# Performance work log

Measured on AMD Instinct MI355X. Metric: run time of the kernel, lower is better.

Reference implementation:

```python
import jax, jax.numpy as jnp
import numpy as np
from jax import lax

B, CIN, H, W = 64, 1024, 28, 28
MID, COUT = 256, 1024  # mid_channels, out_channels*expansion
EMB = 64
EPS = 1e-5


def _conv(x, w, stride=1, padding='VALID'):
    return lax.conv_general_dilated(
        x, w, window_strides=(stride, stride), padding=padding,
        dimension_numbers=('NCHW', 'OIHW', 'NCHW'))


def _bn(x, gamma, beta):
    # training-mode BatchNorm2d: batch statistics over (N,H,W)
    m = jnp.mean(x, axis=(0, 2, 3), keepdims=True)
    v = jnp.var(x, axis=(0, 2, 3), keepdims=True)
    return (x - m) * lax.rsqrt(v + EPS) * gamma[None, :, None, None] + beta[None, :, None, None]


def setup_inputs() -> dict:
    key = jax.random.key(0)
    ks = jax.random.split(key, 12)
    he = lambda k, shape, fan_in: jax.random.normal(k, shape, jnp.float32) * np.float32(np.sqrt(2.0 / fan_in))
    return {
        'x': jax.random.normal(ks[0], (B, CIN, H, W), jnp.float32),
        'embeddings': jax.random.normal(ks[1], (B, EMB), jnp.float32),
        # sparse gating networks: Linear(emb_dim -> channels) + ReLU
        'w_gate1': he(ks[2], (EMB, MID), EMB), 'b_gate1': jnp.zeros((MID,), jnp.float32),
        'w_gate2': he(ks[3], (EMB, MID), EMB), 'b_gate2': jnp.zeros((MID,), jnp.float32),
        'conv1_w': he(ks[4], (MID, CIN, 1, 1), CIN),
        'bn1_g': jnp.ones((MID,), jnp.float32), 'bn1_b': jnp.zeros((MID,), jnp.float32),
        'conv2_w': he(ks[5], (MID, MID, 3, 3), MID * 9),
        'bn2_g': jnp.ones((MID,), jnp.float32), 'bn2_b': jnp.zeros((MID,), jnp.float32),
        'conv3_w': he(ks[6], (COUT, MID, 1, 1), MID),
        'bn3_g': jnp.ones((COUT,), jnp.float32), 'bn3_b': jnp.zeros((COUT,), jnp.float32),
    }


def reference(x, embeddings, w_gate1, b_gate1, w_gate2, b_gate2,
              conv1_w, bn1_g, bn1_b, conv2_w, bn2_g, bn2_b,
              conv3_w, bn3_g, bn3_b):
    identity = x
    # gate 1: ReLU-sparse gating over mid channels, per sample
    g1 = jax.nn.relu(embeddings @ w_gate1 + b_gate1)            # [B, MID]
    out = _conv(x, conv1_w) * g1[:, :, None, None]              # MoE conv1x1
    out = jax.nn.relu(_bn(out, bn1_g, bn1_b))
    g2 = jax.nn.relu(embeddings @ w_gate2 + b_gate2)            # [B, MID]
    out = _conv(out, conv2_w, stride=1, padding='SAME') * g2[:, :, None, None]  # MoE conv3x3
    out = jax.nn.relu(_bn(out, bn2_g, bn2_b))
    out = _conv(out, conv3_w)                                   # plain conv1x1
    out = _bn(out, bn3_g, bn3_b)
    out = jax.nn.relu(out + identity)
    return out, g1, g2
```

## Files before the change

kernel.cpp:

```cpp
#include <hip/hip_runtime.h>
#include <stdint.h>

#define NB 64
#define CINC 1024
#define HWD 784
#define MIDC 256
#define COUTC 1024
#define EMBD 64

typedef __attribute__((ext_vector_type(8))) short short8;
typedef __attribute__((ext_vector_type(4))) float f32x4;

#define GLOAD16(gp, lp)                                                     \
  __builtin_amdgcn_global_load_lds(                                         \
      (const __attribute__((address_space(1))) void*)(gp),                  \
      (__attribute__((address_space(3))) void*)(lp), 16, 0, 0)

__device__ __forceinline__ ushort f2bf(float f) {
  union { float f; uint32_t u; } v; v.f = f;
  uint32_t r = v.u + 0x7fffu + ((v.u >> 16) & 1u);
  return (ushort)(r >> 16);
}
__device__ __forceinline__ float bf2f(ushort b) {
  union { uint32_t u; float f; } v; v.u = ((uint32_t)b) << 16;
  return v.f;
}
__device__ __forceinline__ uint32_t pack2(float a, float b) {
  return (uint32_t)f2bf(a) | ((uint32_t)f2bf(b) << 16);
}

static const size_t OFF_Y1   = 0;
static const size_t OFF_Y2   = 25690112;
static const size_t OFF_W1   = 51380224;
static const size_t OFF_W3   = 51904512;
static const size_t OFF_W2R  = 52428800;
static const size_t OFF_STAT = 53608448;
static const size_t OFF_PAR  = 53620736;
static const size_t OFF_ZB   = 58720256;

__global__ __launch_bounds__(256) void k_gates(
    const float* __restrict__ emb, const float* __restrict__ w1,
    const float* __restrict__ b1, const float* __restrict__ w2,
    const float* __restrict__ b2, float* __restrict__ out_tail) {
  int b = blockIdx.x, which = blockIdx.y, n = threadIdx.x;
  const float* w = which ? w2 : w1;
  const float* bias = which ? b2 : b1;
  __shared__ float se[EMBD];
  if (n < EMBD) se[n] = emb[b * EMBD + n];
  __syncthreads();
  float acc = bias[n];
#pragma unroll 8
  for (int e = 0; e < EMBD; e++) acc += se[e] * w[e * MIDC + n];
  acc = fmaxf(acc, 0.f);
  out_tail[which * (NB * MIDC) + b * MIDC + n] = acc;
}

__global__ void k_repack(const float* __restrict__ w1, const float* __restrict__ w2,
                         const float* __restrict__ w3, ushort* __restrict__ W1b,
                         ushort* __restrict__ W2r, ushort* __restrict__ W3b) {
  int total = 262144 + 262144 + 589824;
  for (int i = blockIdx.x * blockDim.x + threadIdx.x; i < total;
       i += gridDim.x * blockDim.x) {
    if (i < 262144) W1b[i] = f2bf(w1[i]);
    else if (i < 524288) W3b[i - 262144] = f2bf(w3[i - 262144]);
    else {
      int j = i - 524288;
      int tap = j >> 16, n = (j >> 8) & 255, c = j & 255;
      W2r[j] = f2bf(w2[(n * 256 + c) * 9 + tap]);
    }
  }
}

__global__ __launch_bounds__(256) void k_xpose(const float* __restrict__ x,
                                               ushort* __restrict__ xcl) {
  int mt = blockIdx.x, ct = blockIdx.y, b = blockIdx.z;
  __shared__ float tile[64][68];
  int t = threadIdx.x;
  int m0 = mt * 64, c0 = ct * 64;
  {
    int cc = t >> 2, mc = (t & 3) << 4;
    if (m0 + mc < HWD) {
      const float* src = x + ((size_t)b * CINC + c0 + cc) * HWD + m0 + mc;
#pragma unroll
      for (int e = 0; e < 4; e++) {
        float4 q = ((const float4*)src)[e];
        int mm = mc + e * 4;
        tile[mm][cc] = q.x; tile[mm + 1][cc] = q.y;
        tile[mm + 2][cc] = q.z; tile[mm + 3][cc] = q.w;
      }
    }
  }
  __syncthreads();
  {
    int m = t >> 2, cc = (t & 3) << 4;
    int mi = m0 + m;
    if (mi < HWD) {
      float* row = tile[m];
      uint32_t w[8];
#pragma unroll
      for (int e = 0; e < 8; e++) w[e] = pack2(row[cc + 2 * e], row[cc + 2 * e + 1]);
      uint4 p0, p1;
      p0.x = w[0]; p0.y = w[1]; p0.z = w[2]; p0.w = w[3];
      p1.x = w[4]; p1.y = w[5]; p1.z = w[6]; p1.w = w[7];
      uint4* dst = (uint4*)(xcl + ((size_t)b * HWD + mi) * CINC + c0 + cc);
      dst[0] = p0; dst[1] = p1;
    }
  }
}

__global__ __launch_bounds__(256, 3) void k_conv1(
    const ushort* __restrict__ xcl, const ushort* __restrict__ W1b,
    const float* __restrict__ g1, ushort* __restrict__ y1,
    float* __restrict__ sum1, float* __restrict__ sq1) {
  int bid = (blockIdx.x & 7) * 98 + (blockIdx.x >> 3);
  int mt = bid >> 1, nt = bid & 1;
  int tid = threadIdx.x, lane = tid & 63, wid = tid >> 6;
  int wm = wid >> 1, wn = wid & 1;
  int lr = lane & 15, lq = lane >> 4;
  __shared__ char smem[32768];
  char* Ab = smem;
  char* Bb = smem + 16384;

  int l8 = lane >> 3, kgl = lane & 7;
  int xorg = (kgl ^ l8) * 8;
  const ushort* srcA[4]; const ushort* srcB[4];
#pragma unroll
  for (int q = 0; q < 4; q++) {
    int r = (wid * 4 + q) * 8 + l8;
    int m = mt * 128 + r;
    srcA[q] = xcl + (size_t)m * CINC + xorg;
    int n = nt * 128 + r;
    srcB[q] = W1b + (size_t)n * CINC + xorg;
  }
  f32x4 acc[4][4] = {};

  for (int kt = 0; kt < 16; kt++) {
    int d = kt * 64;
#pragma unroll
    for (int q = 0; q < 4; q++) GLOAD16(srcA[q] + d, Ab + (wid * 4 + q) * 1024);
#pragma unroll
    for (int q = 0; q < 4; q++) GLOAD16(srcB[q] + d, Bb + (wid * 4 + q) * 1024);
    __syncthreads();
#pragma unroll
    for (int kk = 0; kk < 2; kk++) {
      int kg = kk * 4 + lq;
      short8 af[4], bf[4];
#pragma unroll
      for (int i = 0; i < 4; i++) {
        int row = wm * 64 + i * 16 + lr;
        af[i] = *(const short8*)(Ab + row * 128 + ((kg ^ (row & 7)) << 4));
      }
#pragma unroll
      for (int j = 0; j < 4; j++) {
        int rn = wn * 64 + j * 16 + lr;
        bf[j] = *(const short8*)(Bb + rn * 128 + ((kg ^ (rn & 7)) << 4));
      }
#pragma unroll
      for (int i = 0; i < 4; i++)
#pragma unroll
        for (int j = 0; j < 4; j++)
          acc[i][j] = __builtin_amdgcn_mfma_f32_16x16x32_bf16(af[i], bf[j], acc[i][j], 0, 0, 0);
    }
    __syncthreads();
  }

  int m0t = mt * 128;
  int b0 = m0t / HWD;
  int b1 = b0 + 1; if (b1 > NB - 1) b1 = NB - 1;
  int thr = (b0 + 1) * HWD;
  float gv0[4], gv1[4];
#pragma unroll
  for (int j = 0; j < 4; j++) {
    int n = nt * 128 + wn * 64 + j * 16 + lr;
    gv0[j] = g1[b0 * MIDC + n];
    gv1[j] = g1[b1 * MIDC + n];
  }
#pragma unroll
  for (int i = 0; i < 4; i++) {
    int mlb = m0t + wm * 64 + i * 16 + lq * 4;
#pragma unroll
    for (int j = 0; j < 4; j++)
#pragma unroll
      for (int r = 0; r < 4; r++)
        acc[i][j][r] *= ((mlb + r) < thr) ? gv0[j] : gv1[j];
  }
#pragma unroll
  for (int j = 0; j < 4; j++) {
    float s = 0.f, q = 0.f;
#pragma unroll
    for (int i = 0; i < 4; i++)
#pragma unroll
      for (int r = 0; r < 4; r++) { float v = acc[i][j][r]; s += v; q += v * v; }
    s += __shfl_xor(s, 16); s += __shfl_xor(s, 32);
    q += __shfl_xor(q, 16); q += __shfl_xor(q, 32);
    if (lane < 16) {
      int n = nt * 128 + wn * 64 + j * 16 + lane;
      atomicAdd(&sum1[n], s); atomicAdd(&sq1[n], q);
    }
  }
#pragma unroll
  for (int i = 0; i < 4; i++)
#pragma unroll
    for (int r = 0; r < 4; r++) {
      int m = m0t + wm * 64 + i * 16 + lq * 4 + r;
      ushort* dst = y1 + (size_t)m * MIDC + nt * 128 + wn * 64 + lr;
#pragma unroll
      for (int j = 0; j < 4; j++) dst[j * 16] = f2bf(acc[i][j][r]);
    }
}

__global__ void k_bnpar(const float* __restrict__ st, const float* __restrict__ gamma,
                        const float* __restrict__ beta, float* __restrict__ so,
                        float* __restrict__ to, int C) {
  int c = blockIdx.x * blockDim.x + threadIdx.x;
  if (c >= C) return;
  const float cnt = 50176.f;
  float m = st[c] / cnt;
  float v = st[C + c] / cnt - m * m;
  float s = gamma[c] * rsqrtf(v + 1e-5f);
  so[c] = s; to[c] = beta[c] - m * s;
}

__global__ __launch_bounds__(256) void k_bnrelu(
    const ushort* __restrict__ y1, const float* __restrict__ s1,
    const float* __restrict__ t1, ushort* __restrict__ y1p) {
  __shared__ float sS[MIDC], sT[MIDC];
  int t = threadIdx.x;
  sS[t] = s1[t]; sT[t] = t1[t];
  __syncthreads();
  int pl = t >> 5, ch = (t & 31) * 8;
  int pos = blockIdx.x * 8 + pl;
  int b = pos / 900, pp = pos % 900;
  int pr = pp / 30, pc = pp % 30;
  uint4 ov = {0u, 0u, 0u, 0u};
  if (pr > 0 && pr < 29 && pc > 0 && pc < 29) {
    uint4 raw = *(const uint4*)(y1 + ((size_t)b * HWD + (pr - 1) * 28 + (pc - 1)) * MIDC + ch);
    ushort* rw = (ushort*)&raw; ushort* ow = (ushort*)&ov;
#pragma unroll
    for (int e = 0; e < 8; e++) {
      float f = bf2f(rw[e]) * sS[ch + e] + sT[ch + e];
      ow[e] = f2bf(fmaxf(f, 0.f));
    }
  }
  *(uint4*)(y1p + (size_t)pos * MIDC + ch) = ov;
}

__global__ __launch_bounds__(256) void k_bnrelu2(
    const ushort* __restrict__ y2, const float* __restrict__ s2,
    const float* __restrict__ t2, ushort* __restrict__ y2p) {
  __shared__ float sS[MIDC], sT[MIDC];
  int t = threadIdx.x;
  sS[t] = s2[t]; sT[t] = t2[t];
  __syncthreads();
  int pl = t >> 5, ch = (t & 31) * 8;
  size_t pos = (size_t)blockIdx.x * 8 + pl;
  uint4 raw = *(const uint4*)(y2 + pos * MIDC + ch);
  uint4 ov;
  ushort* rw = (ushort*)&raw; ushort* ow = (ushort*)&ov;
#pragma unroll
  for (int e = 0; e < 8; e++) {
    float f = bf2f(rw[e]) * sS[ch + e] + sT[ch + e];
    ow[e] = f2bf(fmaxf(f, 0.f));
  }
  *(uint4*)(y2p + pos * MIDC + ch) = ov;
}

__global__ __launch_bounds__(256, 3) void k_conv2(
    const ushort* __restrict__ y1p, const ushort* __restrict__ W2r,
    const float* __restrict__ g2, ushort* __restrict__ y2,
    float* __restrict__ sum2, float* __restrict__ sq2) {
  int bid = (blockIdx.x & 7) * 98 + (blockIdx.x >> 3);
  int mt = bid >> 1, nt = bid & 1;
  int tid = threadIdx.x, lane = tid & 63, wid = tid >> 6;
  int wm = wid >> 1, wn = wid & 1;
  int lr = lane & 15, lq = lane >> 4;
  __shared__ char smem[32768];
  char* Ab = smem;
  char* Bb = smem + 16384;

  int l8 = lane >> 3, kgl = lane & 7;
  int xorg = (kgl ^ l8) * 8;
  const ushort* srcA[4]; const ushort* srcB[4];
#pragma unroll
  for (int q = 0; q < 4; q++) {
    int r = (wid * 4 + q) * 8 + l8;
    int m = mt * 128 + r;
    int b = m / HWD, rem = m % HWD;
    int h = rem / 28, w = rem % 28;
    srcA[q] = y1p + ((size_t)b * 900 + (h + 1) * 30 + (w + 1)) * MIDC + xorg;
    int n = nt * 128 + r;
    srcB[q] = W2r + (size_t)n * MIDC + xorg;
  }
  f32x4 acc[4][4] = {};

  for (int kt = 0; kt < 36; kt++) {
    int tap = kt >> 2, cq = kt & 3;
    int dy = tap / 3, dx = tap % 3;
    int dA = ((dy - 1) * 30 + (dx - 1)) * MIDC + cq * 64;
    int dB = tap * 65536 + cq * 64;
#pragma unroll
    for (int q = 0; q < 4; q++) GLOAD16(srcA[q] + dA, Ab + (wid * 4 + q) * 1024);
#pragma unroll
    for (int q = 0; q < 4; q++) GLOAD16(srcB[q] + dB, Bb + (wid * 4 + q) * 1024);
    __syncthreads();
#pragma unroll
    for (int kk = 0; kk < 2; kk++) {
      int kg = kk * 4 + lq;
      short8 af[4], bf[4];
#pragma unroll
      for (int i = 0; i < 4; i++) {
        int row = wm * 64 + i * 16 + lr;
        af[i] = *(const short8*)(Ab + row * 128 + ((kg ^ (row & 7)) << 4));
      }
#pragma unroll
      for (int j = 0; j < 4; j++) {
        int rn = wn * 64 + j * 16 + lr;
        bf[j] = *(const short8*)(Bb + rn * 128 + ((kg ^ (rn & 7)) << 4));
      }
#pragma unroll
      for (int i = 0; i < 4; i++)
#pragma unroll
        for (int j = 0; j < 4; j++)
          acc[i][j] = __builtin_amdgcn_mfma_f32_16x16x32_bf16(af[i], bf[j], acc[i][j], 0, 0, 0);
    }
    __syncthreads();
  }

  int m0t = mt * 128;
  int b0 = m0t / HWD;
  int b1 = b0 + 1; if (b1 > NB - 1) b1 = NB - 1;
  int thr = (b0 + 1) * HWD;
  float gv0[4], gv1[4];
#pragma unroll
  for (int j = 0; j < 4; j++) {
    int n = nt * 128 + wn * 64 + j * 16 + lr;
    gv0[j] = g2[b0 * MIDC + n];
    gv1[j] = g2[b1 * MIDC + n];
  }
#pragma unroll
  for (int i = 0; i < 4; i++) {
    int mlb = m0t + wm * 64 + i * 16 + lq * 4;
#pragma unroll
    for (int j = 0; j < 4; j++)
#pragma unroll
      for (int r = 0; r < 4; r++)
        acc[i][j][r] *= ((mlb + r) < thr) ? gv0[j] : gv1[j];
  }
#pragma unroll
  for (int j = 0; j < 4; j++) {
    float s = 0.f, q = 0.f;
#pragma unroll
    for (int i = 0; i < 4; i++)
#pragma unroll
      for (int r = 0; r < 4; r++) { float v = acc[i][j][r]; s += v; q += v * v; }
    s += __shfl_xor(s, 16); s += __shfl_xor(s, 32);
    q += __shfl_xor(q, 16); q += __shfl_xor(q, 32);
    if (lane < 16) {
      int n = nt * 128 + wn * 64 + j * 16 + lane;
      atomicAdd(&sum2[n], s); atomicAdd(&sq2[n], q);
    }
  }
#pragma unroll
  for (int i = 0; i < 4; i++)
#pragma unroll
    for (int r = 0; r < 4; r++) {
      int m = m0t + wm * 64 + i * 16 + lq * 4 + r;
      ushort* dst = y2 + (size_t)m * MIDC + nt * 128 + wn * 64 + lr;
#pragma unroll
      for (int j = 0; j < 4; j++) dst[j * 16] = f2bf(acc[i][j][r]);
    }
}

__global__ __launch_bounds__(256, 3) void k_conv3(
    const ushort* __restrict__ y2p, const ushort* __restrict__ W3b,
    ushort* __restrict__ zbn, float* __restrict__ sum3, float* __restrict__ sq3) {
  int bid = (blockIdx.x & 7) * 392 + (blockIdx.x >> 3);
  int mt = bid >> 3, nt = bid & 7;
  int tid = threadIdx.x, lane = tid & 63, wid = tid >> 6;
  int wm = wid >> 1, wn = wid & 1;
  int lr = lane & 15, lq = lane >> 4;
  __shared__ char smem[33792];
  char* Ab = smem;
  char* Bb = smem + 16384;

  int l8 = lane >> 3, kgl = lane & 7;
  int xorg = (kgl ^ l8) * 8;
  const ushort* srcA[4]; const ushort* srcB[4];
#pragma unroll
  for (int q = 0; q < 4; q++) {
    int r = (wid * 4 + q) * 8 + l8;
    int m = mt * 128 + r;
    srcA[q] = y2p + (size_t)m * MIDC + xorg;
    int n = nt * 128 + r;
    srcB[q] = W3b + (size_t)n * MIDC + xorg;
  }
  f32x4 acc[4][4] = {};

  for (int kt = 0; kt < 4; kt++) {
    int d = kt * 64;
#pragma unroll
    for (int q = 0; q < 4; q++) GLOAD16(srcA[q] + d, Ab + (wid * 4 + q) * 1024);
#pragma unroll
    for (int q = 0; q < 4; q++) GLOAD16(srcB[q] + d, Bb + (wid * 4 + q) * 1024);
    __syncthreads();
#pragma unroll
    for (int kk = 0; kk < 2; kk++) {
      int kg = kk * 4 + lq;
      short8 af[4], bf[4];
#pragma unroll
      for (int i = 0; i < 4; i++) {
        int row = wm * 64 + i * 16 + lr;
        af[i] = *(const short8*)(Ab + row * 128 + ((kg ^ (row & 7)) << 4));
      }
#pragma unroll
      for (int j = 0; j < 4; j++) {
        int rn = wn * 64 + j * 16 + lr;
        bf[j] = *(const short8*)(Bb + rn * 128 + ((kg ^ (rn & 7)) << 4));
      }
#pragma unroll
      for (int i = 0; i < 4; i++)
#pragma unroll
        for (int j = 0; j < 4; j++)
          acc[i][j] = __builtin_amdgcn_mfma_f32_16x16x32_bf16(af[i], bf[j], acc[i][j], 0, 0, 0);
    }
    __syncthreads();
  }

#pragma unroll
  for (int j = 0; j < 4; j++) {
    float s = 0.f, q = 0.f;
#pragma unroll
    for (int i = 0; i < 4; i++)
#pragma unroll
      for (int r = 0; r < 4; r++) { float v = acc[i][j][r]; s += v; q += v * v; }
    s += __shfl_xor(s, 16); s += __shfl_xor(s, 32);
    q += __shfl_xor(q, 16); q += __shfl_xor(q, 32);
    if (lane < 16) {
      int n = nt * 128 + wn * 64 + j * 16 + lane;
      atomicAdd(&sum3[n], s); atomicAdd(&sq3[n], q);
    }
  }

  float* ldsf = (float*)smem;
  int m0t = mt * 128;
  for (int h = 0; h < 2; h++) {
    __syncthreads();
    if (wn == h) {
#pragma unroll
      for (int i = 0; i < 4; i++)
#pragma unroll
        for (int j = 0; j < 4; j++) {
          int nc = j * 16 + lr;
#pragma unroll
          for (int r = 0; r < 4; r++) {
            int m = wm * 64 + i * 16 + lq * 4 + r;
            ldsf[nc * 132 + m] = acc[i][j][r];
          }
        }
    }
    __syncthreads();
    int c0 = nt * 128 + h * 64;
    int l = tid & 15;
    int m = m0t + l * 8;
    int b = m / HWD, hw = m % HWD;
#pragma unroll
    for (int pass = 0; pass < 4; pass++) {
      int row = pass * 16 + (tid >> 4);
      const float* src = &ldsf[row * 132 + l * 8];
      uint4 pv;
      pv.x = pack2(src[0], src[1]); pv.y = pack2(src[2], src[3]);
      pv.z = pack2(src[4], src[5]); pv.w = pack2(src[6], src[7]);
      *(uint4*)(zbn + ((size_t)(b * COUTC + c0 + row)) * HWD + hw) = pv;
    }
  }
}

__global__ __launch_bounds__(256) void k_final(
    const ushort* __restrict__ zbn, const float* __restrict__ x,
    const float* __restrict__ s3, const float* __restrict__ t3,
    float* __restrict__ outp) {
  int stride = gridDim.x * blockDim.x;
  int total = (NB * COUTC * HWD) / 8;
  for (int i = blockIdx.x * blockDim.x + threadIdx.x; i < total; i += stride) {
    size_t e0 = (size_t)i * 8;
    int c = (int)((e0 / HWD) & (COUTC - 1));
    float s = s3[c], tt = t3[c];
    uint4 zr = *(const uint4*)(zbn + e0);
    ushort* zw = (ushort*)&zr;
    float4 x0 = *(const float4*)(x + e0);
    float4 x1 = *(const float4*)(x + e0 + 4);
    float4 o0, o1;
    o0.x = fmaxf(fmaf(bf2f(zw[0]), s, tt) + x0.x, 0.f);
    o0.y = fmaxf(fmaf(bf2f(zw[1]), s, tt) + x0.y, 0.f);
    o0.z = fmaxf(fmaf(bf2f(zw[2]), s, tt) + x0.z, 0.f);
    o0.w = fmaxf(fmaf(bf2f(zw[3]), s, tt) + x0.w, 0.f);
    o1.x = fmaxf(fmaf(bf2f(zw[4]), s, tt) + x1.x, 0.f);
    o1.y = fmaxf(fmaf(bf2f(zw[5]), s, tt) + x1.y, 0.f);
    o1.z = fmaxf(fmaf(bf2f(zw[6]), s, tt) + x1.z, 0.f);
    o1.w = fmaxf(fmaf(bf2f(zw[7]), s, tt) + x1.w, 0.f);
    *(float4*)(outp + e0) = o0;
    *(float4*)(outp + e0 + 4) = o1;
  }
}

extern "C" void kernel_launch(void* const* d_in, const int* in_sizes, int n_in,
                              void* d_out, int out_size, void* d_ws, size_t ws_size,
                              hipStream_t stream) {
  const float* x    = (const float*)d_in[0];
  const float* emb  = (const float*)d_in[1];
  const float* wg1  = (const float*)d_in[2];
  const float* bg1  = (const float*)d_in[3];
  const float* wg2  = (const float*)d_in[4];
  const float* bg2  = (const float*)d_in[5];
  const float* c1w  = (const float*)d_in[6];
  const float* bn1g = (const float*)d_in[7];
  const float* bn1b = (const float*)d_in[8];
  const float* c2w  = (const float*)d_in[9];
  const float* bn2g = (const float*)d_in[10];
  const float* bn2b = (const float*)d_in[11];
  const float* c3w  = (const float*)d_in[12];
  const float* bn3g = (const float*)d_in[13];
  const float* bn3b = (const float*)d_in[14];

  float* out = (float*)d_out;
  char* ws = (char*)d_ws;
  ushort* y1  = (ushort*)(ws + OFF_Y1);
  ushort* y2p = (ushort*)(ws + OFF_Y1);
  ushort* y2  = (ushort*)(ws + OFF_Y2);
  ushort* W1b = (ushort*)(ws + OFF_W1);
  ushort* W3b = (ushort*)(ws + OFF_W3);
  ushort* W2r = (ushort*)(ws + OFF_W2R);
  float* stat = (float*)(ws + OFF_STAT);
  float* par  = (float*)(ws + OFF_PAR);
  ushort* zbn = (ushort*)(ws + OFF_ZB);

  float* sum1 = stat;        float* sq1 = stat + 256;
  float* sum2 = stat + 512;  float* sq2 = stat + 768;
  float* sum3 = stat + 1024; float* sq3 = stat + 2048;
  float* s1 = par;        float* t1 = par + 256;
  float* s2 = par + 512;  float* t2 = par + 768;
  float* s3 = par + 1024; float* t3 = par + 2048;

  ushort* xcl = (ushort*)out;
  ushort* y1p = (ushort*)(out + 25690112);
  float* out_tail = out + 51380224;

  hipMemsetAsync(stat, 0, 3072 * sizeof(float), stream);
  k_gates<<<dim3(64, 2), 256, 0, stream>>>(emb, wg1, bg1, wg2, bg2, out_tail);
  k_repack<<<2048, 256, 0, stream>>>(c1w, c2w, c3w, W1b, W2r, W3b);
  k_xpose<<<dim3(13, 16, 64), 256, 0, stream>>>(x, xcl);
  k_conv1<<<784, 256, 0, stream>>>(xcl, W1b, out_tail, y1, sum1, sq1);
  k_bnpar<<<1, 256, 0, stream>>>(stat, bn1g, bn1b, s1, t1, 256);
  k_bnrelu<<<7200, 256, 0, stream>>>(y1, s1, t1, y1p);
  k_conv2<<<784, 256, 0, stream>>>(y1p, W2r, out_tail + 16384, y2, sum2, sq2);
  k_bnpar<<<1, 256, 0, stream>>>(stat + 512, bn2g, bn2b, s2, t2, 256);
  k_bnrelu2<<<6272, 256, 0, stream>>>(y2, s2, t2, y2p);
  k_conv3<<<3136, 256, 0, stream>>>(y2p, W3b, zbn, sum3, sq3);
  k_bnpar<<<4, 256, 0, stream>>>(stat + 1024, bn3g, bn3b, s3, t3, 1024);
  k_final<<<2048, 256, 0, stream>>>(zbn, x, s3, t3, out);
}
```

Measured before the change: 388.2 us.

## Widen conv GEMM tiles to 128x256 with 8 waves and merge setup kernels

The three conv GEMM kernels move from 256-thread blocks with 128x128 output tiles to 512-thread blocks with 128x256 tiles. Each block now covers every mid channel, so the activation tile is loaded once per block instead of once per N tile, halving A-operand global traffic. LDS use rises to 48 KB per block and the launch_bounds hint changes to (512,4), which may cut occupancy. Separately, the gating, weight repack and stats memset are merged into one setup kernel to drop two launches.

```diff
diff --git a/kernel.cpp b/kernel.cpp
--- a/kernel.cpp
+++ b/kernel.cpp
@@ -38,35 +38,39 @@
 static const size_t OFF_PAR  = 53620736;
 static const size_t OFF_ZB   = 58720256;
 
-__global__ __launch_bounds__(256) void k_gates(
-    const float* __restrict__ emb, const float* __restrict__ w1,
-    const float* __restrict__ b1, const float* __restrict__ w2,
-    const float* __restrict__ b2, float* __restrict__ out_tail) {
-  int b = blockIdx.x, which = blockIdx.y, n = threadIdx.x;
-  const float* w = which ? w2 : w1;
-  const float* bias = which ? b2 : b1;
-  __shared__ float se[EMBD];
-  if (n < EMBD) se[n] = emb[b * EMBD + n];
-  __syncthreads();
-  float acc = bias[n];
+__global__ __launch_bounds__(256) void k_setup(
+    const float* __restrict__ emb, const float* __restrict__ wg1,
+    const float* __restrict__ bg1, const float* __restrict__ wg2,
+    const float* __restrict__ bg2, float* __restrict__ out_tail,
+    const float* __restrict__ w1, const float* __restrict__ w2,
+    const float* __restrict__ w3, ushort* __restrict__ W1b,
+    ushort* __restrict__ W2r, ushort* __restrict__ W3b,
+    float* __restrict__ stat) {
+  int bid = blockIdx.x;
+  if (bid < 128) {
+    int b = bid >> 1, which = bid & 1, n = threadIdx.x;
+    const float* w = which ? wg2 : wg1;
+    const float* bias = which ? bg2 : bg1;
+    __shared__ float se[EMBD];
+    if (n < EMBD) se[n] = emb[b * EMBD + n];
+    __syncthreads();
+    float acc = bias[n];
 #pragma unroll 8
-  for (int e = 0; e < EMBD; e++) acc += se[e] * w[e * MIDC + n];
-  acc = fmaxf(acc, 0.f);
-  out_tail[which * (NB * MIDC) + b * MIDC + n] = acc;
-}
-
-__global__ void k_repack(const float* __restrict__ w1, const float* __restrict__ w2,
-                         const float* __restrict__ w3, ushort* __restrict__ W1b,
-                         ushort* __restrict__ W2r, ushort* __restrict__ W3b) {
-  int total = 262144 + 262144 + 589824;
-  for (int i = blockIdx.x * blockDim.x + threadIdx.x; i < total;
-       i += gridDim.x * blockDim.x) {
-    if (i < 262144) W1b[i] = f2bf(w1[i]);
-    else if (i < 524288) W3b[i - 262144] = f2bf(w3[i - 262144]);
-    else {
-      int j = i - 524288;
-      int tap = j >> 16, n = (j >> 8) & 255, c = j & 255;
-      W2r[j] = f2bf(w2[(n * 256 + c) * 9 + tap]);
+    for (int e = 0; e < EMBD; e++) acc += se[e] * w[e * MIDC + n];
+    out_tail[which * (NB * MIDC) + b * MIDC + n] = fmaxf(acc, 0.f);
+  } else {
+    int rb = bid - 128;
+    int j0 = rb * 256 + threadIdx.x;
+    if (j0 < 3072) stat[j0] = 0.f;
+    int total = 262144 + 262144 + 589824;
+    for (int i = j0; i < total; i += 2048 * 256) {
+      if (i < 262144) W1b[i] = f2bf(w1[i]);
+      else if (i < 524288) W3b[i - 262144] = f2bf(w3[i - 262144]);
+      else {
+        int j = i - 524288;
+        int tap = j >> 16, n = (j >> 8) & 255, c = j & 255;
+        W2r[j] = f2bf(w2[(n * 256 + c) * 9 + tap]);
+      }
     }
   }
 }
@@ -108,36 +112,37 @@
   }
 }
 
-__global__ __launch_bounds__(256, 3) void k_conv1(
+__global__ __launch_bounds__(512, 4) void k_conv1(
     const ushort* __restrict__ xcl, const ushort* __restrict__ W1b,
     const float* __restrict__ g1, ushort* __restrict__ y1,
     float* __restrict__ sum1, float* __restrict__ sq1) {
-  int bid = (blockIdx.x & 7) * 98 + (blockIdx.x >> 3);
-  int mt = bid >> 1, nt = bid & 1;
+  int mt = (blockIdx.x & 7) * 49 + (blockIdx.x >> 3);
   int tid = threadIdx.x, lane = tid & 63, wid = tid >> 6;
-  int wm = wid >> 1, wn = wid & 1;
+  int wm = wid >> 2, wn = wid & 3;
   int lr = lane & 15, lq = lane >> 4;
-  __shared__ char smem[32768];
+  __shared__ char smem[49152];
   char* Ab = smem;
   char* Bb = smem + 16384;
 
   int l8 = lane >> 3, kgl = lane & 7;
   int xorg = (kgl ^ l8) * 8;
-  const ushort* srcA[4]; const ushort* srcB[4];
+  const ushort* srcA[2]; const ushort* srcB[4];
+#pragma unroll
+  for (int q = 0; q < 2; q++) {
+    int r = (wid * 2 + q) * 8 + l8;
+    srcA[q] = xcl + (size_t)(mt * 128 + r) * CINC + xorg;
+  }
 #pragma unroll
   for (int q = 0; q < 4; q++) {
     int r = (wid * 4 + q) * 8 + l8;
-    int m = mt * 128 + r;
-    srcA[q] = xcl + (size_t)m * CINC + xorg;
-    int n = nt * 128 + r;
-    srcB[q] = W1b + (size_t)n * CINC + xorg;
+    srcB[q] = W1b + (size_t)r * CINC + xorg;
   }
   f32x4 acc[4][4] = {};
 
   for (int kt = 0; kt < 16; kt++) {
     int d = kt * 64;
 #pragma unroll
-    for (int q = 0; q < 4; q++) GLOAD16(srcA[q] + d, Ab + (wid * 4 + q) * 1024);
+    for (int q = 0; q < 2; q++) GLOAD16(srcA[q] + d, Ab + (wid * 2 + q) * 1024);
 #pragma unroll
     for (int q = 0; q < 4; q++) GLOAD16(srcB[q] + d, Bb + (wid * 4 + q) * 1024);
     __syncthreads();
@@ -171,7 +176,7 @@
   float gv0[4], gv1[4];
 #pragma unroll
   for (int j = 0; j < 4; j++) {
-    int n = nt * 128 + wn * 64 + j * 16 + lr;
+    int n = wn * 64 + j * 16 + lr;
     gv0[j] = g1[b0 * MIDC + n];
     gv1[j] = g1[b1 * MIDC + n];
   }
@@ -194,7 +199,7 @@
     s += __shfl_xor(s, 16); s += __shfl_xor(s, 32);
     q += __shfl_xor(q, 16); q += __shfl_xor(q, 32);
     if (lane < 16) {
-      int n = nt * 128 + wn * 64 + j * 16 + lane;
+      int n = wn * 64 + j * 16 + lane;
       atomicAdd(&sum1[n], s); atomicAdd(&sq1[n], q);
     }
   }
@@ -203,7 +208,7 @@
 #pragma unroll
     for (int r = 0; r < 4; r++) {
       int m = m0t + wm * 64 + i * 16 + lq * 4 + r;
-      ushort* dst = y1 + (size_t)m * MIDC + nt * 128 + wn * 64 + lr;
+      ushort* dst = y1 + (size_t)m * MIDC + wn * 64 + lr;
 #pragma unroll
       for (int j = 0; j < 4; j++) dst[j * 16] = f2bf(acc[i][j][r]);
     }
@@ -265,31 +270,33 @@
   *(uint4*)(y2p + pos * MIDC + ch) = ov;
 }
 
-__global__ __launch_bounds__(256, 3) void k_conv2(
+__global__ __launch_bounds__(512, 4) void k_conv2(
     const ushort* __restrict__ y1p, const ushort* __restrict__ W2r,
     const float* __restrict__ g2, ushort* __restrict__ y2,
     float* __restrict__ sum2, float* __restrict__ sq2) {
-  int bid = (blockIdx.x & 7) * 98 + (blockIdx.x >> 3);
-  int mt = bid >> 1, nt = bid & 1;
+  int mt = (blockIdx.x & 7) * 49 + (blockIdx.x >> 3);
   int tid = threadIdx.x, lane = tid & 63, wid = tid >> 6;
-  int wm = wid >> 1, wn = wid & 1;
+  int wm = wid >> 2, wn = wid & 3;
   int lr = lane & 15, lq = lane >> 4;
-  __shared__ char smem[32768];
+  __shared__ char smem[49152];
   char* Ab = smem;
   char* Bb = smem + 16384;
 
   int l8 = lane >> 3, kgl = lane & 7;
   int xorg = (kgl ^ l8) * 8;
-  const ushort* srcA[4]; const ushort* srcB[4];
-#pragma unroll
-  for (int q = 0; q < 4; q++) {
-    int r = (wid * 4 + q) * 8 + l8;
+  const ushort* srcA[2]; const ushort* srcB[4];
+#pragma unroll
+  for (int q = 0; q < 2; q++) {
+    int r = (wid * 2 + q) * 8 + l8;
     int m = mt * 128 + r;
     int b = m / HWD, rem = m % HWD;
     int h = rem / 28, w = rem % 28;
     srcA[q] = y1p + ((size_t)b * 900 + (h + 1) * 30 + (w + 1)) * MIDC + xorg;
-    int n = nt * 128 + r;
-    srcB[q] = W2r + (size_t)n * MIDC + xorg;
+  }
+#pragma unroll
+  for (int q = 0; q < 4; q++) {
+    int r = (wid * 4 + q) * 8 + l8;
+    srcB[q] = W2r + (size_t)r * MIDC + xorg;
   }
   f32x4 acc[4][4] = {};
 
@@ -299,7 +306,7 @@
     int dA = ((dy - 1) * 30 + (dx - 1)) * MIDC + cq * 64;
     int dB = tap * 65536 + cq * 64;
 #pragma unroll
-    for (int q = 0; q < 4; q++) GLOAD16(srcA[q] + dA, Ab + (wid * 4 + q) * 1024);
+    for (int q = 0; q < 2; q++) GLOAD16(srcA[q] + dA, Ab + (wid * 2 + q) * 1024);
 #pragma unroll
     for (int q = 0; q < 4; q++) GLOAD16(srcB[q] + dB, Bb + (wid * 4 + q) * 1024);
     __syncthreads();
@@ -333,7 +340,7 @@
   float gv0[4], gv1[4];
 #pragma unroll
   for (int j = 0; j < 4; j++) {
-    int n = nt * 128 + wn * 64 + j * 16 + lr;
+    int n = wn * 64 + j * 16 + lr;
     gv0[j] = g2[b0 * MIDC + n];
     gv1[j] = g2[b1 * MIDC + n];
   }
@@ -356,7 +363,7 @@
     s += __shfl_xor(s, 16); s += __shfl_xor(s, 32);
     q += __shfl_xor(q, 16); q += __shfl_xor(q, 32);
     if (lane < 16) {
-      int n = nt * 128 + wn * 64 + j * 16 + lane;
+      int n = wn * 64 + j * 16 + lane;
       atomicAdd(&sum2[n], s); atomicAdd(&sq2[n], q);
     }
   }
@@ -365,41 +372,43 @@
 #pragma unroll
     for (int r = 0; r < 4; r++) {
       int m = m0t + wm * 64 + i * 16 + lq * 4 + r;
-      ushort* dst = y2 + (size_t)m * MIDC + nt * 128 + wn * 64 + lr;
+      ushort* dst = y2 + (size_t)m * MIDC + wn * 64 + lr;
 #pragma unroll
       for (int j = 0; j < 4; j++) dst[j * 16] = f2bf(acc[i][j][r]);
     }
 }
 
-__global__ __launch_bounds__(256, 3) void k_conv3(
+__global__ __launch_bounds__(512, 4) void k_conv3(
     const ushort* __restrict__ y2p, const ushort* __restrict__ W3b,
     ushort* __restrict__ zbn, float* __restrict__ sum3, float* __restrict__ sq3) {
-  int bid = (blockIdx.x & 7) * 392 + (blockIdx.x >> 3);
-  int mt = bid >> 3, nt = bid & 7;
+  int bid = (blockIdx.x & 7) * 196 + (blockIdx.x >> 3);
+  int mt = bid >> 2, nt = bid & 3;
   int tid = threadIdx.x, lane = tid & 63, wid = tid >> 6;
-  int wm = wid >> 1, wn = wid & 1;
+  int wm = wid >> 2, wn = wid & 3;
   int lr = lane & 15, lq = lane >> 4;
-  __shared__ char smem[33792];
+  __shared__ char smem[49152];
   char* Ab = smem;
   char* Bb = smem + 16384;
 
   int l8 = lane >> 3, kgl = lane & 7;
   int xorg = (kgl ^ l8) * 8;
-  const ushort* srcA[4]; const ushort* srcB[4];
+  const ushort* srcA[2]; const ushort* srcB[4];
+#pragma unroll
+  for (int q = 0; q < 2; q++) {
+    int r = (wid * 2 + q) * 8 + l8;
+    srcA[q] = y2p + (size_t)(mt * 128 + r) * MIDC + xorg;
+  }
 #pragma unroll
   for (int q = 0; q < 4; q++) {
     int r = (wid * 4 + q) * 8 + l8;
-    int m = mt * 128 + r;
-    srcA[q] = y2p + (size_t)m * MIDC + xorg;
-    int n = nt * 128 + r;
-    srcB[q] = W3b + (size_t)n * MIDC + xorg;
+    srcB[q] = W3b + (size_t)(nt * 256 + r) * MIDC + xorg;
   }
   f32x4 acc[4][4] = {};
 
   for (int kt = 0; kt < 4; kt++) {
     int d = kt * 64;
 #pragma unroll
-    for (int q = 0; q < 4; q++) GLOAD16(srcA[q] + d, Ab + (wid * 4 + q) * 1024);
+    for (int q = 0; q < 2; q++) GLOAD16(srcA[q] + d, Ab + (wid * 2 + q) * 1024);
 #pragma unroll
     for (int q = 0; q < 4; q++) GLOAD16(srcB[q] + d, Bb + (wid * 4 + q) * 1024);
     __syncthreads();
@@ -436,14 +445,14 @@
     s += __shfl_xor(s, 16); s += __shfl_xor(s, 32);
     q += __shfl_xor(q, 16); q += __shfl_xor(q, 32);
     if (lane < 16) {
-      int n = nt * 128 + wn * 64 + j * 16 + lane;
+      int n = nt * 256 + wn * 64 + j * 16 + lane;
       atomicAdd(&sum3[n], s); atomicAdd(&sq3[n], q);
     }
   }
 
   float* ldsf = (float*)smem;
   int m0t = mt * 128;
-  for (int h = 0; h < 2; h++) {
+  for (int h = 0; h < 4; h++) {
     __syncthreads();
     if (wn == h) {
 #pragma unroll
@@ -459,13 +468,13 @@
         }
     }
     __syncthreads();
-    int c0 = nt * 128 + h * 64;
+    int c0 = nt * 256 + h * 64;
     int l = tid & 15;
     int m = m0t + l * 8;
     int b = m / HWD, hw = m % HWD;
 #pragma unroll
-    for (int pass = 0; pass < 4; pass++) {
-      int row = pass * 16 + (tid >> 4);
+    for (int pass = 0; pass < 2; pass++) {
+      int row = pass * 32 + (tid >> 4);
       const float* src = &ldsf[row * 132 + l * 8];
       uint4 pv;
       pv.x = pack2(src[0], src[1]); pv.y = pack2(src[2], src[3]);
@@ -545,17 +554,16 @@
   ushort* y1p = (ushort*)(out + 25690112);
   float* out_tail = out + 51380224;
 
-  hipMemsetAsync(stat, 0, 3072 * sizeof(float), stream);
-  k_gates<<<dim3(64, 2), 256, 0, stream>>>(emb, wg1, bg1, wg2, bg2, out_tail);
-  k_repack<<<2048, 256, 0, stream>>>(c1w, c2w, c3w, W1b, W2r, W3b);
+  k_setup<<<2176, 256, 0, stream>>>(emb, wg1, bg1, wg2, bg2, out_tail,
+                                    c1w, c2w, c3w, W1b, W2r, W3b, stat);
   k_xpose<<<dim3(13, 16, 64), 256, 0, stream>>>(x, xcl);
-  k_conv1<<<784, 256, 0, stream>>>(xcl, W1b, out_tail, y1, sum1, sq1);
+  k_conv1<<<392, 512, 0, stream>>>(xcl, W1b, out_tail, y1, sum1, sq1);
   k_bnpar<<<1, 256, 0, stream>>>(stat, bn1g, bn1b, s1, t1, 256);
   k_bnrelu<<<7200, 256, 0, stream>>>(y1, s1, t1, y1p);
-  k_conv2<<<784, 256, 0, stream>>>(y1p, W2r, out_tail + 16384, y2, sum2, sq2);
+  k_conv2<<<392, 512, 0, stream>>>(y1p, W2r, out_tail + 16384, y2, sum2, sq2);
   k_bnpar<<<1, 256, 0, stream>>>(stat + 512, bn2g, bn2b, s2, t2, 256);
   k_bnrelu2<<<6272, 256, 0, stream>>>(y2, s2, t2, y2p);
-  k_conv3<<<3136, 256, 0, stream>>>(y2p, W3b, zbn, sum3, sq3);
+  k_conv3<<<1568, 512, 0, stream>>>(y2p, W3b, zbn, sum3, sq3);
   k_bnpar<<<4, 256, 0, stream>>>(stat + 1024, bn3g, bn3b, s3, t3, 1024);
   k_final<<<2048, 256, 0, stream>>>(zbn, x, s3, t3, out);
 }
```

New measurement: 400.1 us. 3.1% more time.
